# Performance work log

Hardware: AMD Instinct MI355X
Metric: run time of the kernel (lower is better)

The kernel has to match this reference:

```python
import math
import jax, jax.numpy as jnp
import numpy as np

GROUPS = 8

def setup_inputs() -> dict:
    key = jax.random.key(0)
    ks = jax.random.split(key, 6)
    N, H, W, C = 8, 128, 128, 512
    s = 1.0 / math.sqrt(C)
    return {
        "x": jax.random.normal(ks[0], (N, H, W, C), dtype=jnp.float32),
        "Wq": jax.random.normal(ks[1], (C, C), dtype=jnp.float32) * s,
        "Wk": jax.random.normal(ks[2], (C, C), dtype=jnp.float32) * s,
        "Wv": jax.random.normal(ks[3], (C, C), dtype=jnp.float32) * s,
        "Wo": jax.random.normal(ks[4], (C, C), dtype=jnp.float32) * s,
        "bo": jnp.zeros((C,), dtype=jnp.float32),
    }

def reference(x, Wq, Wk, Wv, Wo, bo):
    # width=False: attend along H axis -> permute to [N, W, H, C]
    x = jnp.transpose(x, (0, 2, 1, 3))
    N, W, H, C = x.shape
    g = GROUPS
    gp = C // g  # group_planes (head dim)
    xr = x.reshape(N * W, H, C)
    # torch nn.Linear: y = x @ W^T
    q = (xr @ Wq.T).reshape(N * W, H, g, gp)
    k = (xr @ Wk.T).reshape(N * W, H, g, gp)
    v = (xr @ Wv.T).reshape(N * W, H, g, gp)
    attn = jnp.einsum('nigc,njgc->nijg', q, k / math.sqrt(gp))
    attn = jax.nn.softmax(attn, axis=2)
    out = jnp.einsum('nijg,njgc->nigc', attn, v)
    out = out.reshape(N * W, H, C)
    out = out @ Wo.T + bo
    out = out.reshape(N, W, H, C)
    return jnp.transpose(out, (0, 2, 1, 3))
```

## Files before the change

### kernel.cpp

```cpp
#include <hip/hip_runtime.h>
#include <stdint.h>


typedef __attribute__((ext_vector_type(4))) float f32x4;
typedef __attribute__((ext_vector_type(8))) short bf16x8;
typedef unsigned short u16;
typedef unsigned int u32;

#define CBAR() asm volatile("" ::: "memory")
#define SBAR() do { CBAR(); __builtin_amdgcn_s_barrier(); CBAR(); } while(0)
#define LGKM0() do { asm volatile("s_waitcnt lgkmcnt(0)" ::: "memory"); __builtin_amdgcn_sched_barrier(0); } while(0)
#define VMC(n) asm volatile("s_waitcnt vmcnt(" #n ")" ::: "memory")

static __device__ __forceinline__ u16 f2bf(float f){
    union { float f; u32 u; } v; v.f = f;
    u32 r = v.u + 0x7fffu + ((v.u >> 16) & 1u);
    return (u16)(r >> 16);
}

static __device__ __forceinline__ void gload16(const void* g, void* l){
    __builtin_amdgcn_global_load_lds((const __attribute__((address_space(1))) void*)g,
                                     (__attribute__((address_space(3))) void*)l, 16, 0, 0);
}

__global__ void k_wconv(const float* __restrict__ Wq, const float* __restrict__ Wk,
                        const float* __restrict__ Wv, const float* __restrict__ Wo,
                        u16* __restrict__ Wcat, u16* __restrict__ Wob){
    int e = (blockIdx.x * 256 + threadIdx.x) * 4;
    if (e < 1536*512) {
        int row = e >> 9, col = e & 511;
        const float* s = (row < 512) ? (Wq + row*512)
                        : (row < 1024 ? Wk + (row-512)*512 : Wv + (row-1024)*512);
        float4 v = *(const float4*)(s + col);
        ushort4 o = { f2bf(v.x), f2bf(v.y), f2bf(v.z), f2bf(v.w) };
        *(ushort4*)(Wcat + e) = o;
    } else {
        int e2 = e - 1536*512;
        float4 v = *(const float4*)(Wo + e2);
        ushort4 o = { f2bf(v.x), f2bf(v.y), f2bf(v.z), f2bf(v.w) };
        *(ushort4*)(Wob + e2) = o;
    }
}

__global__ void k_xconv(const float* __restrict__ x, u16* __restrict__ xb, int n0){
    int t = blockIdx.x * 256 + threadIdx.x;
    int ml = t >> 6;
    int c0 = (t & 63) << 3;
    int nl = ml >> 7, h = ml & 127;
    int n = n0 + nl, nb = n >> 7, w = n & 127;
    const float* src = x + (size_t)((nb*128 + h)*128 + w) * 512 + c0;
    float4 a = *(const float4*)(src);
    float4 b = *(const float4*)(src + 4);
    uint4 o;
    o.x = (u32)f2bf(a.x) | ((u32)f2bf(a.y) << 16);
    o.y = (u32)f2bf(a.z) | ((u32)f2bf(a.w) << 16);
    o.z = (u32)f2bf(b.x) | ((u32)f2bf(b.y) << 16);
    o.w = (u32)f2bf(b.z) | ((u32)f2bf(b.w) << 16);
    *(uint4*)(xb + (size_t)ml*512 + c0) = o;
}

template<int NCOL, bool OUTPROJ>
__global__ __launch_bounds__(512, 4) void k_gemm3(const u16* __restrict__ A, const u16* __restrict__ B,
                                                  void* __restrict__ Cout, const float* __restrict__ bias,
                                                  int n0, int nrow, int planesz){
    extern __shared__ char smc[];
    const int tid = threadIdx.x;
    const int wid = tid >> 6, lane = tid & 63, lg = lane >> 4, li = lane & 15;
    const int wr = wid >> 1, wc = wid & 1;
    const int bid = blockIdx.x;
    const int xcd = bid & 7, l = bid >> 3;
    const int row_tile = xcd * (nrow >> 3) + l / NCOL;
    const int col_tile = l % NCOL;
    const int m0 = row_tile * 256, nn0 = col_tile * 128;

    auto stage = [&](int s, int kb){
        char* sl = smc + s*24576;
        #pragma unroll
        for (int i = 0; i < 2; ++i) {
            int R = wid*32 + i*16;
            int r = R + (lane >> 2);
            int cq = (lane & 3) ^ ((r >> 1) & 3);
            gload16((const char*)(A + (size_t)(m0 + r)*512 + kb) + cq*16, sl + R*64);
        }
        int rb = wid*16 + (lane >> 2);
        int cqb = (lane & 3) ^ ((rb >> 1) & 3);
        gload16((const char*)(B + (size_t)(nn0 + rb)*512 + kb) + cqb*16, sl + 16384 + wid*1024);
    };

    f32x4 acc[4][4];
    #pragma unroll
    for (int i = 0; i < 4; ++i)
        #pragma unroll
        for (int j = 0; j < 4; ++j)
            acc[i][j] = f32x4{0.f, 0.f, 0.f, 0.f};

    stage(0, 0);
    stage(1, 32);
    VMC(3);
    SBAR();

    for (int t = 0; t < 16; ++t) {
        const int sc = t % 3;
        char* sl = smc + sc*24576;

        if (t < 14) stage((sc + 2) % 3, (t + 2) * 32);

        bf16x8 af[4], bfr[4];
        #pragma unroll
        for (int f = 0; f < 4; ++f) {
            int ra = wr*64 + f*16 + li;
            af[f] = *(const bf16x8*)(sl + ra*64 + (((lg ^ (ra >> 1)) & 3) << 4));
        }
        #pragma unroll
        for (int f = 0; f < 4; ++f) {
            int rb = wc*64 + f*16 + li;
            bfr[f] = *(const bf16x8*)(sl + 16384 + rb*64 + (((lg ^ (rb >> 1)) & 3) << 4));
        }

        LGKM0();
        __builtin_amdgcn_s_setprio(1);
        #pragma unroll
        for (int fi = 0; fi < 4; ++fi)
            #pragma unroll
            for (int fj = 0; fj < 4; ++fj)
                acc[fi][fj] = __builtin_amdgcn_mfma_f32_16x16x32_bf16(af[fi], bfr[fj], acc[fi][fj], 0, 0, 0);
        __builtin_amdgcn_s_setprio(0);

        if (t < 13) { VMC(3); } else { VMC(0); }
        SBAR();
    }

    if (!OUTPROJ) {
        u16* Cp = (u16*)Cout + (size_t)(nn0 >> 9) * planesz;
        const int cb = (nn0 & 511) + wc*64;
        #pragma unroll
        for (int fi = 0; fi < 4; ++fi)
            #pragma unroll
            for (int fj = 0; fj < 4; ++fj)
                #pragma unroll
                for (int r = 0; r < 4; ++r) {
                    int row = m0 + wr*64 + fi*16 + lg*4 + r;
                    int col = cb + fj*16 + li;
                    Cp[(size_t)row*512 + col] = f2bf(acc[fi][fj][r]);
                }
    } else {
        float* C = (float*)Cout;
        #pragma unroll
        for (int fi = 0; fi < 4; ++fi)
            #pragma unroll
            for (int fj = 0; fj < 4; ++fj)
                #pragma unroll
                for (int r = 0; r < 4; ++r) {
                    int row = m0 + wr*64 + fi*16 + lg*4 + r;
                    int col = nn0 + wc*64 + fj*16 + li;
                    int mg = n0*128 + row;
                    int n = mg >> 7, ii = mg & 127;
                    int nb = n >> 7, w = n & 127;
                    C[(size_t)((nb*128 + ii)*128 + w) * 512 + col] = acc[fi][fj][r] + bias[col];
                }
    }
}

__global__ __launch_bounds__(256, 2) void k_attn(const u16* __restrict__ Qpl, const u16* __restrict__ Kpl,
                                                 const u16* __restrict__ Vpl, u16* __restrict__ Ob){
    __shared__ char sm[52224];
    const int g = blockIdx.x;
    const int nl = blockIdx.y;
    const int tid = threadIdx.x;
    const int wid = tid >> 6, lane = tid & 63, lg = lane >> 4, li = lane & 15;

    const u16* Qg = Qpl + (size_t)nl*128*512 + g*64;
    const u16* Kg = Kpl + (size_t)nl*128*512 + g*64;
    const u16* Vg = Vpl + (size_t)nl*128*512 + g*64;
    u16*       Og = Ob  + (size_t)nl*128*512 + g*64;

    #pragma unroll
    for (int it = 0; it < 4; ++it) {
        int gi = it*256 + tid;
        int row = gi >> 3, gs = gi & 7;
        int sw = (gs ^ (row & 7)) << 4;
        gload16((const char*)(Qg + (size_t)row*512) + sw, sm + it*4096 + wid*1024);
        gload16((const char*)(Kg + (size_t)row*512) + sw, sm + 16384 + it*4096 + wid*1024);
    }
    {
        int j = tid & 127, ch = tid >> 7;
        const u16* src = Vg + (size_t)j*512 + ch*32;
        uint4 a0 = *(const uint4*)(src);
        uint4 a1 = *(const uint4*)(src + 8);
        uint4 a2 = *(const uint4*)(src + 16);
        uint4 a3 = *(const uint4*)(src + 24);
        u32 w[16] = {a0.x,a0.y,a0.z,a0.w, a1.x,a1.y,a1.z,a1.w,
                     a2.x,a2.y,a2.z,a2.w, a3.x,a3.y,a3.z,a3.w};
        char* dst = sm + 34816 + ch*32*272 + j*2;
        #pragma unroll
        for (int cc = 0; cc < 32; ++cc) {
            u32 word = w[cc >> 1];
            u16 val = (cc & 1) ? (u16)(word >> 16) : (u16)(word & 0xffffu);
            *(u16*)(dst + cc*272) = val;
        }
    }
    __syncthreads();

    const int i0w = wid*32;
    f32x4 s[2][8];
    #pragma unroll
    for (int t = 0; t < 2; ++t)
        #pragma unroll
        for (int tj = 0; tj < 8; ++tj)
            s[t][tj] = f32x4{0.f,0.f,0.f,0.f};

    #pragma unroll
    for (int ks = 0; ks < 2; ++ks) {
        bf16x8 qf[2];
        #pragma unroll
        for (int t = 0; t < 2; ++t) {
            int ra = i0w + t*16 + li;
            qf[t] = *(const bf16x8*)(sm + ra*128 + ((ks*64 + lg*16) ^ ((ra & 7) << 4)));
        }
        #pragma unroll
        for (int tj = 0; tj < 8; ++tj) {
            int rb = tj*16 + li;
            bf16x8 kf = *(const bf16x8*)(sm + 16384 + rb*128 + ((ks*64 + lg*16) ^ ((rb & 7) << 4)));
            #pragma unroll
            for (int t = 0; t < 2; ++t)
                s[t][tj] = __builtin_amdgcn_mfma_f32_16x16x32_bf16(qf[t], kf, s[t][tj], 0, 0, 0);
        }
    }
    __syncthreads();

    char* pb = sm + wid*8704;
    #pragma unroll
    for (int t = 0; t < 2; ++t) {
        #pragma unroll
        for (int r = 0; r < 4; ++r) {
            float mx = -1e30f;
            #pragma unroll
            for (int tj = 0; tj < 8; ++tj) mx = fmaxf(mx, s[t][tj][r]);
            #pragma unroll
            for (int off = 1; off < 16; off <<= 1) mx = fmaxf(mx, __shfl_xor(mx, off, 64));
            float p[8]; float sum = 0.f;
            #pragma unroll
            for (int tj = 0; tj < 8; ++tj) { p[tj] = __expf((s[t][tj][r] - mx)*0.125f); sum += p[tj]; }
            #pragma unroll
            for (int off = 1; off < 16; off <<= 1) sum += __shfl_xor(sum, off, 64);
            float inv = 1.0f / sum;
            int prow = t*16 + lg*4 + r;
            #pragma unroll
            for (int tj = 0; tj < 8; ++tj)
                *(u16*)(pb + prow*272 + (tj*16 + li)*2) = f2bf(p[tj]*inv);
        }
    }

    f32x4 o[2][4];
    #pragma unroll
    for (int t = 0; t < 2; ++t)
        #pragma unroll
        for (int tc = 0; tc < 4; ++tc)
            o[t][tc] = f32x4{0.f,0.f,0.f,0.f};

    #pragma unroll
    for (int ks = 0; ks < 4; ++ks) {
        bf16x8 pf[2];
        #pragma unroll
        for (int t = 0; t < 2; ++t)
            pf[t] = *(const bf16x8*)(pb + (t*16 + li)*272 + (ks*64 + lg*16));
        #pragma unroll
        for (int tc = 0; tc < 4; ++tc) {
            bf16x8 vf = *(const bf16x8*)(sm + 34816 + (tc*16 + li)*272 + (ks*64 + lg*16));
            #pragma unroll
            for (int t = 0; t < 2; ++t)
                o[t][tc] = __builtin_amdgcn_mfma_f32_16x16x32_bf16(pf[t], vf, o[t][tc], 0, 0, 0);
        }
    }

    #pragma unroll
    for (int t = 0; t < 2; ++t)
        #pragma unroll
        for (int tc = 0; tc < 4; ++tc)
            #pragma unroll
            for (int r = 0; r < 4; ++r) {
                int irow = i0w + t*16 + lg*4 + r;
                int col = tc*16 + li;
                Og[(size_t)irow*512 + col] = f2bf(o[t][tc][r]);
            }
}

extern "C" void kernel_launch(void* const* d_in, const int* in_sizes, int n_in,
                              void* d_out, int out_size, void* d_ws, size_t ws_size,
                              hipStream_t stream){
    const float* x  = (const float*)d_in[0];
    const float* Wq = (const float*)d_in[1];
    const float* Wk = (const float*)d_in[2];
    const float* Wv = (const float*)d_in[3];
    const float* Wo = (const float*)d_in[4];
    const float* bo = (const float*)d_in[5];

    char* ws = (char*)d_ws;
    u16* Wcat = (u16*)ws;
    u16* Wob  = Wcat + 1536*512;

    int CN = 1024;
    while (CN > 64 && (size_t)2097152 + (size_t)CN*524288 > ws_size) CN >>= 1;
    u16* xb   = (u16*)(ws + 2097152);
    u16* QKV2 = xb + (size_t)CN*128*512;
    int planesz = CN*128*512;

    hipFuncSetAttribute((const void*)&k_gemm3<12, false>,
                        hipFuncAttributeMaxDynamicSharedMemorySize, 73728);
    hipFuncSetAttribute((const void*)&k_gemm3<4, true>,
                        hipFuncAttributeMaxDynamicSharedMemorySize, 73728);

    k_wconv<<<1024, 256, 0, stream>>>(Wq, Wk, Wv, Wo, Wcat, Wob);
    int nch = 1024 / CN;
    for (int ch = 0; ch < nch; ++ch) {
        int n0 = ch * CN;
        int nrow = (CN * 128) / 256;
        k_xconv<<<CN*32, 256, 0, stream>>>(x, xb, n0);
        k_gemm3<12, false><<<nrow*12, 512, 73728, stream>>>(xb, Wcat, QKV2, nullptr, 0, nrow, planesz);
        k_attn<<<dim3(8, CN), 256, 0, stream>>>(QKV2, QKV2 + planesz, QKV2 + 2*(size_t)planesz, xb);
        k_gemm3<4, true ><<<nrow*4,  512, 73728, stream>>>(xb, Wob, d_out, bo, n0, nrow, 0);
    }
}
```

Baseline: 643.2 us.

## Enlarge GEMM tile to 256x256 with 4-stage split A/B pipeline

Replaces the 256x128-tile projection GEMM with a 256x256 tile in which each wave computes 128x64, doubling accumulators. A and B staging are split and interleaved between two half-step MFMA phases over a 4-deep LDS ring buffer of 128 KB. The aim is to raise arithmetic intensity per LDS and global load and to hide load latency better. In exchange, register pressure is higher, occupancy drops to 2 blocks per CU, and there are more barriers per k-step.

```diff
diff --git a/kernel.cpp b/kernel.cpp
--- a/kernel.cpp
+++ b/kernel.cpp
@@ -60,21 +60,22 @@
 }
 
 template<int NCOL, bool OUTPROJ>
-__global__ __launch_bounds__(512, 4) void k_gemm3(const u16* __restrict__ A, const u16* __restrict__ B,
+__global__ __launch_bounds__(512, 2) void k_gemm4(const u16* __restrict__ A, const u16* __restrict__ B,
                                                   void* __restrict__ Cout, const float* __restrict__ bias,
                                                   int n0, int nrow, int planesz){
     extern __shared__ char smc[];
     const int tid = threadIdx.x;
     const int wid = tid >> 6, lane = tid & 63, lg = lane >> 4, li = lane & 15;
-    const int wr = wid >> 1, wc = wid & 1;
+    const int wm = wid >> 2, wn = wid & 3;
     const int bid = blockIdx.x;
     const int xcd = bid & 7, l = bid >> 3;
     const int row_tile = xcd * (nrow >> 3) + l / NCOL;
     const int col_tile = l % NCOL;
-    const int m0 = row_tile * 256, nn0 = col_tile * 128;
-
-    auto stage = [&](int s, int kb){
-        char* sl = smc + s*24576;
+    const int m0 = row_tile * 256, nn0 = col_tile * 256;
+
+    auto stageA = [&](int st){
+        char* sl = smc + (st & 3)*32768;
+        const int kb = st*32;
         #pragma unroll
         for (int i = 0; i < 2; ++i) {
             int R = wid*32 + i*16;
@@ -82,42 +83,48 @@
             int cq = (lane & 3) ^ ((r >> 1) & 3);
             gload16((const char*)(A + (size_t)(m0 + r)*512 + kb) + cq*16, sl + R*64);
         }
-        int rb = wid*16 + (lane >> 2);
-        int cqb = (lane & 3) ^ ((rb >> 1) & 3);
-        gload16((const char*)(B + (size_t)(nn0 + rb)*512 + kb) + cqb*16, sl + 16384 + wid*1024);
     };
-
-    f32x4 acc[4][4];
-    #pragma unroll
-    for (int i = 0; i < 4; ++i)
+    auto stageB = [&](int st){
+        char* sl = smc + (st & 3)*32768 + 16384;
+        const int kb = st*32;
+        #pragma unroll
+        for (int i = 0; i < 2; ++i) {
+            int R = wid*32 + i*16;
+            int r = R + (lane >> 2);
+            int cq = (lane & 3) ^ ((r >> 1) & 3);
+            gload16((const char*)(B + (size_t)(nn0 + r)*512 + kb) + cq*16, sl + R*64);
+        }
+    };
+
+    f32x4 acc[8][4];
+    #pragma unroll
+    for (int i = 0; i < 8; ++i)
         #pragma unroll
         for (int j = 0; j < 4; ++j)
             acc[i][j] = f32x4{0.f, 0.f, 0.f, 0.f};
 
-    stage(0, 0);
-    stage(1, 32);
-    VMC(3);
+    stageA(0); stageB(0);
+    stageA(1); stageB(1);
+    stageA(2); stageB(2);
+    VMC(8);
     SBAR();
 
+    bf16x8 af[4], bfr[4];
     for (int t = 0; t < 16; ++t) {
-        const int sc = t % 3;
-        char* sl = smc + sc*24576;
-
-        if (t < 14) stage((sc + 2) % 3, (t + 2) * 32);
-
-        bf16x8 af[4], bfr[4];
+        char* sl = smc + (t & 3)*32768;
+
         #pragma unroll
         for (int f = 0; f < 4; ++f) {
-            int ra = wr*64 + f*16 + li;
+            int ra = wm*128 + f*16 + li;
             af[f] = *(const bf16x8*)(sl + ra*64 + (((lg ^ (ra >> 1)) & 3) << 4));
         }
         #pragma unroll
         for (int f = 0; f < 4; ++f) {
-            int rb = wc*64 + f*16 + li;
+            int rb = wn*64 + f*16 + li;
             bfr[f] = *(const bf16x8*)(sl + 16384 + rb*64 + (((lg ^ (rb >> 1)) & 3) << 4));
         }
-
-        LGKM0();
+        if (t < 13) stageA(t + 3);
+        SBAR(); LGKM0();
         __builtin_amdgcn_s_setprio(1);
         #pragma unroll
         for (int fi = 0; fi < 4; ++fi)
@@ -125,38 +132,55 @@
             for (int fj = 0; fj < 4; ++fj)
                 acc[fi][fj] = __builtin_amdgcn_mfma_f32_16x16x32_bf16(af[fi], bfr[fj], acc[fi][fj], 0, 0, 0);
         __builtin_amdgcn_s_setprio(0);
-
-        if (t < 13) { VMC(3); } else { VMC(0); }
+        SBAR();
+
+        #pragma unroll
+        for (int f = 0; f < 4; ++f) {
+            int ra = wm*128 + (4 + f)*16 + li;
+            af[f] = *(const bf16x8*)(sl + ra*64 + (((lg ^ (ra >> 1)) & 3) << 4));
+        }
+        if (t < 13) stageB(t + 3);
+        SBAR(); LGKM0();
+        __builtin_amdgcn_s_setprio(1);
+        #pragma unroll
+        for (int fi = 0; fi < 4; ++fi)
+            #pragma unroll
+            for (int fj = 0; fj < 4; ++fj)
+                acc[4 + fi][fj] = __builtin_amdgcn_mfma_f32_16x16x32_bf16(af[fi], bfr[fj], acc[4 + fi][fj], 0, 0, 0);
+        __builtin_amdgcn_s_setprio(0);
+        if (t < 13)      { VMC(8); }
+        else if (t == 13){ VMC(4); }
+        else if (t == 14){ VMC(0); }
         SBAR();
     }
 
     if (!OUTPROJ) {
         u16* Cp = (u16*)Cout + (size_t)(nn0 >> 9) * planesz;
-        const int cb = (nn0 & 511) + wc*64;
-        #pragma unroll
-        for (int fi = 0; fi < 4; ++fi)
-            #pragma unroll
-            for (int fj = 0; fj < 4; ++fj)
+        const int cb = (nn0 & 511) + wn*64;
+        #pragma unroll
+        for (int mf = 0; mf < 8; ++mf)
+            #pragma unroll
+            for (int nf = 0; nf < 4; ++nf)
                 #pragma unroll
                 for (int r = 0; r < 4; ++r) {
-                    int row = m0 + wr*64 + fi*16 + lg*4 + r;
-                    int col = cb + fj*16 + li;
-                    Cp[(size_t)row*512 + col] = f2bf(acc[fi][fj][r]);
+                    int row = m0 + wm*128 + mf*16 + lg*4 + r;
+                    int col = cb + nf*16 + li;
+                    Cp[(size_t)row*512 + col] = f2bf(acc[mf][nf][r]);
                 }
     } else {
         float* C = (float*)Cout;
         #pragma unroll
-        for (int fi = 0; fi < 4; ++fi)
-            #pragma unroll
-            for (int fj = 0; fj < 4; ++fj)
+        for (int mf = 0; mf < 8; ++mf)
+            #pragma unroll
+            for (int nf = 0; nf < 4; ++nf)
                 #pragma unroll
                 for (int r = 0; r < 4; ++r) {
-                    int row = m0 + wr*64 + fi*16 + lg*4 + r;
-                    int col = nn0 + wc*64 + fj*16 + li;
+                    int row = m0 + wm*128 + mf*16 + lg*4 + r;
+                    int col = nn0 + wn*64 + nf*16 + li;
                     int mg = n0*128 + row;
                     int n = mg >> 7, ii = mg & 127;
                     int nb = n >> 7, w = n & 127;
-                    C[(size_t)((nb*128 + ii)*128 + w) * 512 + col] = acc[fi][fj][r] + bias[col];
+                    C[(size_t)((nb*128 + ii)*128 + w) * 512 + col] = acc[mf][nf][r] + bias[col];
                 }
     }
 }
@@ -305,10 +329,10 @@
     u16* QKV2 = xb + (size_t)CN*128*512;
     int planesz = CN*128*512;
 
-    hipFuncSetAttribute((const void*)&k_gemm3<12, false>,
-                        hipFuncAttributeMaxDynamicSharedMemorySize, 73728);
-    hipFuncSetAttribute((const void*)&k_gemm3<4, true>,
-                        hipFuncAttributeMaxDynamicSharedMemorySize, 73728);
+    hipFuncSetAttribute((const void*)&k_gemm4<6, false>,
+                        hipFuncAttributeMaxDynamicSharedMemorySize, 131072);
+    hipFuncSetAttribute((const void*)&k_gemm4<2, true>,
+                        hipFuncAttributeMaxDynamicSharedMemorySize, 131072);
 
     k_wconv<<<1024, 256, 0, stream>>>(Wq, Wk, Wv, Wo, Wcat, Wob);
     int nch = 1024 / CN;
@@ -316,8 +340,8 @@
         int n0 = ch * CN;
         int nrow = (CN * 128) / 256;
         k_xconv<<<CN*32, 256, 0, stream>>>(x, xb, n0);
-        k_gemm3<12, false><<<nrow*12, 512, 73728, stream>>>(xb, Wcat, QKV2, nullptr, 0, nrow, planesz);
+        k_gemm4<6, false><<<nrow*6, 512, 131072, stream>>>(xb, Wcat, QKV2, nullptr, 0, nrow, planesz);
         k_attn<<<dim3(8, CN), 256, 0, stream>>>(QKV2, QKV2 + planesz, QKV2 + 2*(size_t)planesz, xb);
-        k_gemm3<4, true ><<<nrow*4,  512, 73728, stream>>>(xb, Wob, d_out, bo, n0, nrow, 0);
-    }
-}
+        k_gemm4<2, true ><<<nrow*2, 512, 131072, stream>>>(xb, Wob, d_out, bo, n0, nrow, 0);
+    }
+}
```

After: 632.2 us. No clear change (-1.7%).
